# Performance work log

Measured on AMD Instinct MI355X. Metric: run time of the kernel, lower is better.

The kernel has to match this reference:

```python
import jax, jax.numpy as jnp
import numpy as np

EMBED = 1024
HEAD = 128
B, T = 4, 4096


def setup_inputs() -> dict:
    key = jax.random.key(0)
    k1, k2, k3, k4 = jax.random.split(key, 4)
    context = jax.random.normal(k1, (B, T, EMBED), dtype=jnp.float32)
    # nn.Linear(embedding_size, head_size, bias=False): y = x @ W^T; store W^T as [C, H]
    s = 1.0 / np.sqrt(EMBED)
    Wk = jax.random.normal(k2, (EMBED, HEAD), dtype=jnp.float32) * s
    Wq = jax.random.normal(k3, (EMBED, HEAD), dtype=jnp.float32) * s
    Wv = jax.random.normal(k4, (EMBED, HEAD), dtype=jnp.float32) * s
    return {"context": context, "Wk": Wk, "Wq": Wq, "Wv": Wv}


def reference(context, Wk, Wq, Wv):
    Bc, Tc, C = context.shape
    k = jnp.einsum("btc,ch->bth", context, Wk)
    q = jnp.einsum("btc,ch->bth", context, Wq)
    v = jnp.einsum("btc,ch->bth", context, Wv)
    # NOTE: original scales by 1/sqrt(C) (embedding size), not 1/sqrt(head_size)
    scale = 1.0 / jnp.sqrt(jnp.float32(C))
    scores = jnp.einsum("bqh,bkh->bqk", q, k) * scale  # [B, T, T]
    causal = jnp.tril(jnp.ones((Tc, Tc), dtype=bool))
    scores = jnp.where(causal, scores, -jnp.inf)
    attn = jax.nn.softmax(scores, axis=-1)
    # dropout_rate = 0.0 (eval-mode): no-op
    out = jnp.einsum("bqk,bkh->bqh", attn, v)
    return out
```

## Files before the change

### kernel.cpp

```cpp
#include <hip/hip_runtime.h>
#include <cstdint>
#include <cstddef>

#define EMBED 1024
#define HEAD  128
#define BATCH 4
#define SEQ   4096
#define KSC   0.04508422f

typedef __attribute__((ext_vector_type(4))) float f32x4;
typedef __attribute__((ext_vector_type(16))) float f32x16;
typedef __attribute__((ext_vector_type(8))) short s16x8;
typedef __attribute__((ext_vector_type(4))) int i32x4;
typedef __attribute__((ext_vector_type(4))) unsigned short u16x4;

__device__ __forceinline__ unsigned short f2bf(float f) {
    union { float f; unsigned u; } v; v.f = f;
    unsigned r = v.u + 0x7fffu + ((v.u >> 16) & 1u);
    return (unsigned short)(r >> 16);
}

__device__ __forceinline__ int cvtpk(float lo, float hi_) {
    int r;
    asm("v_cvt_pk_bf16_f32 %0, %1, %2" : "=v"(r) : "v"(lo), "v"(hi_));
    return r;
}

__global__ __launch_bounds__(256) void wt_kernel(const float* __restrict__ Wq,
                                                 const float* __restrict__ Wk,
                                                 const float* __restrict__ Wv,
                                                 unsigned short* __restrict__ Wt) {
    int idx = blockIdx.x * 256 + threadIdx.x;
    int sel = idx >> 17;
    int r   = idx & 131071;
    const float* W = (sel == 0) ? Wq : (sel == 1) ? Wk : Wv;
    int h = r >> 10, k = r & 1023;
    Wt[(size_t)(sel * 128 + h) * EMBED + k] = f2bf(W[(size_t)k * HEAD + h]);
}

__global__ __launch_bounds__(256) void proj_kernel(const float* __restrict__ ctx,
                                                   const unsigned short* __restrict__ Wt,
                                                   unsigned short* __restrict__ QKV) {
    __shared__ __align__(16) short As[128 * 72];
    __shared__ __align__(16) short Bs[128 * 72];
    const int tid = threadIdx.x;
    const int lane = tid & 63, w = tid >> 6;
    const int wr = w >> 1, wc = w & 1;
    const int lr = lane & 15, lk = lane >> 4;
    const int m0 = blockIdx.x * 128;
    const unsigned short* Wts = Wt + (size_t)blockIdx.y * 131072;
    unsigned short* outp = QKV + (size_t)blockIdx.y * 2097152;

    f32x4 zero = {0.f, 0.f, 0.f, 0.f};
    f32x4 acc[4][4];
    #pragma unroll
    for (int i = 0; i < 4; ++i)
        #pragma unroll
        for (int jn = 0; jn < 4; ++jn) acc[i][jn] = zero;

    for (int kk = 0; kk < EMBED; kk += 64) {
        __syncthreads();
        #pragma unroll
        for (int t = 0; t < 4; ++t) {
            int c = tid + t * 256;
            int row = c >> 3, cg = c & 7;
            const float* src = ctx + (size_t)(m0 + row) * EMBED + kk + cg * 8;
            f32x4 x0 = *(const f32x4*)src;
            f32x4 x1 = *(const f32x4*)(src + 4);
            s16x8 cv;
            cv[0] = (short)f2bf(x0[0]); cv[1] = (short)f2bf(x0[1]);
            cv[2] = (short)f2bf(x0[2]); cv[3] = (short)f2bf(x0[3]);
            cv[4] = (short)f2bf(x1[0]); cv[5] = (short)f2bf(x1[1]);
            cv[6] = (short)f2bf(x1[2]); cv[7] = (short)f2bf(x1[3]);
            *(s16x8*)&As[row * 72 + cg * 8] = cv;
            *(s16x8*)&Bs[row * 72 + cg * 8] =
                *(const s16x8*)(Wts + (size_t)row * EMBED + kk + cg * 8);
        }
        __syncthreads();
        s16x8 af[4][2], bfr[4][2];
        #pragma unroll
        for (int mi = 0; mi < 4; ++mi)
            #pragma unroll
            for (int k2 = 0; k2 < 2; ++k2)
                af[mi][k2] = *(const s16x8*)&As[(wr * 64 + mi * 16 + lr) * 72 + k2 * 32 + lk * 8];
        #pragma unroll
        for (int ni = 0; ni < 4; ++ni)
            #pragma unroll
            for (int k2 = 0; k2 < 2; ++k2)
                bfr[ni][k2] = *(const s16x8*)&Bs[(wc * 64 + ni * 16 + lr) * 72 + k2 * 32 + lk * 8];
        #pragma unroll
        for (int k2 = 0; k2 < 2; ++k2)
            #pragma unroll
            for (int mi = 0; mi < 4; ++mi)
                #pragma unroll
                for (int ni = 0; ni < 4; ++ni)
                    acc[mi][ni] = __builtin_amdgcn_mfma_f32_16x16x32_bf16(af[mi][k2], bfr[ni][k2], acc[mi][ni], 0, 0, 0);
    }
    #pragma unroll
    for (int mi = 0; mi < 4; ++mi) {
        int row = m0 + wr * 64 + mi * 16 + lk * 4;
        #pragma unroll
        for (int ni = 0; ni < 4; ++ni) {
            int col = wc * 64 + ni * 16 + lr;
            #pragma unroll
            for (int r = 0; r < 4; ++r)
                outp[(size_t)(row + r) * HEAD + col] = f2bf(acc[mi][ni][r]);
        }
    }
}

__global__ __launch_bounds__(256) void vt_kernel(const unsigned short* __restrict__ V,
                                                 unsigned short* __restrict__ Vt) {
    __shared__ __align__(16) unsigned short L[64][136];
    const int tid = threadIdx.x;
    const int t0 = blockIdx.x * 64;
    const int b  = t0 >> 12;
    const int tl = t0 & (SEQ - 1);
    #pragma unroll
    for (int j = 0; j < 4; ++j) {
        int c = tid + j * 256;
        int row = c >> 4, cg = c & 15;
        *(s16x8*)&L[row][cg * 8] =
            *(const s16x8*)(V + (size_t)(t0 + row) * HEAD + cg * 8);
    }
    __syncthreads();
    #pragma unroll
    for (int j = 0; j < 4; ++j) {
        int c = tid + j * 256;
        int h = c >> 3, tg = c & 7;
        s16x8 y;
        #pragma unroll
        for (int e = 0; e < 8; ++e) y[e] = (short)L[tg * 8 + e][h];
        *(s16x8*)(Vt + ((size_t)b * HEAD + h) * SEQ + tl + tg * 8) = y;
    }
}

__global__ __launch_bounds__(256, 2) void attn_kernel(const unsigned short* __restrict__ Q,
                                                      const unsigned short* __restrict__ K,
                                                      const unsigned short* __restrict__ Vt,
                                                      unsigned short* __restrict__ po,
                                                      float* __restrict__ pml) {
    __shared__ __align__(16) char smem[32768];
    const int tid = threadIdx.x;
    const int lane = tid & 63, w = tid >> 6;
    const int l31 = lane & 31, hi = lane >> 5;
    const int hi16 = hi << 4;

    const int b = blockIdx.x / 272;
    int t = blockIdx.x % 272;
    int qt = 0, cum = 0;
    while (cum + ((qt >> 1) + 1) <= t) { cum += (qt >> 1) + 1; ++qt; }
    const int c = t - cum;
    const int nj = min(4, 2 * qt + 2 - 4 * c);
    const int kb0 = c * 256;
    const int slot = b * 272 + cum + c;

    const unsigned short* qp = Q + ((size_t)(b * SEQ + qt * 128 + w * 32 + l31)) * HEAD + hi * 8;
    s16x8 qf[8];
    #pragma unroll
    for (int dt = 0; dt < 8; ++dt) qf[dt] = *(const s16x8*)(qp + dt * 16);

    f32x16 o0, o1, o2, o3;
    #pragma unroll
    for (int r = 0; r < 16; ++r) { o0[r] = 0.f; o1[r] = 0.f; o2[r] = 0.f; o3[r] = 0.f; }
    float m_run = -1e30f, l_run = 0.f;

    const int krow = tid >> 4, kch = tid & 15;
    const int vdr  = tid >> 3, vch = tid & 7;

    s16x8 kst[4], vst[4];
    #pragma unroll
    for (int p = 0; p < 4; ++p) {
        kst[p] = *(const s16x8*)(K + ((size_t)(b * SEQ + kb0 + krow + p * 16)) * HEAD + kch * 8);
        vst[p] = *(const s16x8*)(Vt + ((size_t)(b * HEAD + vdr + p * 32)) * SEQ + kb0 + vch * 8);
    }
    #pragma unroll
    for (int p = 0; p < 4; ++p) {
        int r0 = krow + p * 16;
        *(s16x8*)(smem + r0 * 256 + ((kch * 16) ^ ((r0 & 7) << 4))) = kst[p];
        int d0 = vdr + p * 32;
        *(s16x8*)(smem + 16384 + d0 * 128 + ((vch * 16) ^ ((d0 & 7) << 4))) = vst[p];
    }
    __syncthreads();

    for (int j = 0; j < nj; ++j) {
        const int kb = kb0 + j * 64;
        if (j + 1 < nj) {
            int kbn = kb + 64;
            #pragma unroll
            for (int p = 0; p < 4; ++p) {
                kst[p] = *(const s16x8*)(K + ((size_t)(b * SEQ + kbn + krow + p * 16)) * HEAD + kch * 8);
                vst[p] = *(const s16x8*)(Vt + ((size_t)(b * HEAD + vdr + p * 32)) * SEQ + kbn + vch * 8);
            }
        }

        f32x16 st0, st1;
        #pragma unroll
        for (int r = 0; r < 16; ++r) { st0[r] = 0.f; st1[r] = 0.f; }
        const int sw = (l31 & 7) << 4;
        const char* kbase0 = smem + l31 * 256;
        const char* kbase1 = kbase0 + 32 * 256;
        __builtin_amdgcn_s_setprio(1);
        #pragma unroll
        for (int dt = 0; dt < 8; ++dt) {
            s16x8 ka0 = *(const s16x8*)(kbase0 + ((dt * 32 + hi16) ^ sw));
            s16x8 ka1 = *(const s16x8*)(kbase1 + ((dt * 32 + hi16) ^ sw));
            st0 = __builtin_amdgcn_mfma_f32_32x32x16_bf16(ka0, qf[dt], st0, 0, 0, 0);
            st1 = __builtin_amdgcn_mfma_f32_32x32x16_bf16(ka1, qf[dt], st1, 0, 0, 0);
        }
        __builtin_amdgcn_s_setprio(0);

        if (4 * c + j >= 2 * qt) {
            const int qg = qt * 128 + w * 32 + l31;
            #pragma unroll
            for (int r = 0; r < 16; ++r) {
                int crow = (r & 3) + 8 * (r >> 2) + 4 * hi;
                if (kb + crow > qg)      st0[r] = -3e37f;
                if (kb + 32 + crow > qg) st1[r] = -3e37f;
            }
        }

        float mx = st0[0];
        #pragma unroll
        for (int r = 1; r < 16; ++r) mx = fmaxf(mx, st0[r]);
        #pragma unroll
        for (int r = 0; r < 16; ++r) mx = fmaxf(mx, st1[r]);
        mx = fmaxf(mx, __shfl_xor(mx, 32));
        float mt = mx * KSC;
        if (!__all(mt <= m_run + 8.0f)) {
            float mn = fmaxf(m_run, mt);
            float f = exp2f(m_run - mn);
            l_run *= f;
            int fi = __float_as_int(f);
            #pragma unroll
            for (int r = 0; r < 16; ++r) {
                int srcb = 4 * ((r & 3) + 8 * (r >> 2)) + 16 * hi;
                float fr = __int_as_float(__builtin_amdgcn_ds_bpermute(srcb, fi));
                o0[r] *= fr; o1[r] *= fr; o2[r] *= fr; o3[r] *= fr;
            }
            m_run = mn;
        }
        float rs = 0.f;
        #pragma unroll
        for (int r = 0; r < 16; ++r) {
            st0[r] = exp2f(fmaf(st0[r], KSC, -m_run)); rs += st0[r];
            st1[r] = exp2f(fmaf(st1[r], KSC, -m_run)); rs += st1[r];
        }
        rs += __shfl_xor(rs, 32);
        l_run += rs;

        int a0 = cvtpk(st0[0], st0[1]),   b0 = cvtpk(st0[4], st0[5]);
        int a1 = cvtpk(st0[2], st0[3]),   b1 = cvtpk(st0[6], st0[7]);
        int a2 = cvtpk(st0[8], st0[9]),   b2 = cvtpk(st0[12], st0[13]);
        int a3 = cvtpk(st0[10], st0[11]), b3 = cvtpk(st0[14], st0[15]);
        int a4 = cvtpk(st1[0], st1[1]),   b4 = cvtpk(st1[4], st1[5]);
        int a5 = cvtpk(st1[2], st1[3]),   b5 = cvtpk(st1[6], st1[7]);
        int a6 = cvtpk(st1[8], st1[9]),   b6 = cvtpk(st1[12], st1[13]);
        int a7 = cvtpk(st1[10], st1[11]), b7 = cvtpk(st1[14], st1[15]);
        asm volatile("v_permlane32_swap_b32 %0, %1" : "+v"(a0), "+v"(b0));
        asm volatile("v_permlane32_swap_b32 %0, %1" : "+v"(a1), "+v"(b1));
        asm volatile("v_permlane32_swap_b32 %0, %1" : "+v"(a2), "+v"(b2));
        asm volatile("v_permlane32_swap_b32 %0, %1" : "+v"(a3), "+v"(b3));
        asm volatile("v_permlane32_swap_b32 %0, %1" : "+v"(a4), "+v"(b4));
        asm volatile("v_permlane32_swap_b32 %0, %1" : "+v"(a5), "+v"(b5));
        asm volatile("v_permlane32_swap_b32 %0, %1" : "+v"(a6), "+v"(b6));
        asm volatile("v_permlane32_swap_b32 %0, %1" : "+v"(a7), "+v"(b7));
        i32x4 pw0 = {a0, a1, b0, b1}; s16x8 pa0 = *(s16x8*)&pw0;
        i32x4 pw1 = {a2, a3, b2, b3}; s16x8 pa1 = *(s16x8*)&pw1;
        i32x4 pw2 = {a4, a5, b4, b5}; s16x8 pa2 = *(s16x8*)&pw2;
        i32x4 pw3 = {a6, a7, b6, b7}; s16x8 pa3 = *(s16x8*)&pw3;

        __builtin_amdgcn_s_setprio(1);
        #define PV_NT(oo, nt) { \
            const int vr = (nt) * 32 + l31; \
            const int vsw = (vr & 7) << 4; \
            const char* vb = smem + 16384 + vr * 128; \
            oo = __builtin_amdgcn_mfma_f32_32x32x16_bf16(pa0, *(const s16x8*)(vb + ((0  + hi16) ^ vsw)), oo, 0, 0, 0); \
            oo = __builtin_amdgcn_mfma_f32_32x32x16_bf16(pa1, *(const s16x8*)(vb + ((32 + hi16) ^ vsw)), oo, 0, 0, 0); \
            oo = __builtin_amdgcn_mfma_f32_32x32x16_bf16(pa2, *(const s16x8*)(vb + ((64 + hi16) ^ vsw)), oo, 0, 0, 0); \
            oo = __builtin_amdgcn_mfma_f32_32x32x16_bf16(pa3, *(const s16x8*)(vb + ((96 + hi16) ^ vsw)), oo, 0, 0, 0); }
        PV_NT(o0, 0) PV_NT(o1, 1) PV_NT(o2, 2) PV_NT(o3, 3)
        #undef PV_NT
        __builtin_amdgcn_s_setprio(0);

        if (j + 1 < nj) {
            __syncthreads();
            #pragma unroll
            for (int p = 0; p < 4; ++p) {
                int r0 = krow + p * 16;
                *(s16x8*)(smem + r0 * 256 + ((kch * 16) ^ ((r0 & 7) << 4))) = kst[p];
                int d0 = vdr + p * 32;
                *(s16x8*)(smem + 16384 + d0 * 128 + ((vch * 16) ^ ((d0 & 7) << 4))) = vst[p];
            }
            __syncthreads();
        }
    }

    unsigned short* pob = po + (size_t)slot * 16384;
    #define STORE_NT(oo, nt) { \
        _Pragma("unroll") \
        for (int r = 0; r < 16; ++r) { \
            int qin = w * 32 + (r & 3) + 8 * (r >> 2) + 4 * hi; \
            pob[qin * 128 + (nt) * 32 + l31] = f2bf(oo[r]); \
        } }
    STORE_NT(o0, 0) STORE_NT(o1, 1) STORE_NT(o2, 2) STORE_NT(o3, 3)
    #undef STORE_NT
    if (lane < 32) {
        float* pm = pml + (size_t)slot * 256 + (w * 32 + lane) * 2;
        pm[0] = m_run; pm[1] = l_run;
    }
}

__global__ __launch_bounds__(256) void combine_kernel(const unsigned short* __restrict__ po,
                                                      const float* __restrict__ pml,
                                                      float* __restrict__ out) {
    const int tid = threadIdx.x;
    const int row = blockIdx.x * 8 + (tid >> 5);
    const int l32 = tid & 31;
    const int b = row >> 12, q = row & 4095;
    const int qt = q >> 7, qr = q & 127;
    const int nc = (q >> 8) + 1;
    const int cum = ((qt >> 1) + (qt & 1)) * ((qt >> 1) + 1);
    const size_t bslot = (size_t)b * 272 + cum;

    float M = -1e30f;
    for (int cc = 0; cc < nc; ++cc)
        M = fmaxf(M, pml[(bslot + cc) * 256 + qr * 2]);
    float L = 0.f;
    f32x4 acc = {0.f, 0.f, 0.f, 0.f};
    for (int cc = 0; cc < nc; ++cc) {
        const float* pm = pml + (bslot + cc) * 256 + qr * 2;
        float wgt = exp2f(pm[0] - M);
        L += wgt * pm[1];
        u16x4 x = *(const u16x4*)(po + (bslot + cc) * 16384 + qr * 128 + l32 * 4);
        #pragma unroll
        for (int e = 0; e < 4; ++e) {
            union { unsigned u; float f; } cv; cv.u = ((unsigned)x[e]) << 16;
            acc[e] += wgt * cv.f;
        }
    }
    float inv = 1.f / L;
    f32x4 y = {acc[0] * inv, acc[1] * inv, acc[2] * inv, acc[3] * inv};
    *(f32x4*)(out + (size_t)row * HEAD + l32 * 4) = y;
}

extern "C" void kernel_launch(void* const* d_in, const int* in_sizes, int n_in,
                              void* d_out, int out_size, void* d_ws, size_t ws_size,
                              hipStream_t stream) {
    const float* ctx = (const float*)d_in[0];
    const float* Wk  = (const float*)d_in[1];
    const float* Wq  = (const float*)d_in[2];
    const float* Wv  = (const float*)d_in[3];
    float* out = (float*)d_out;

    unsigned short* Wt  = (unsigned short*)d_ws;
    unsigned short* Qb  = Wt + 3 * 131072;
    unsigned short* Kb  = Qb + 2097152;
    unsigned short* Vb  = Kb + 2097152;
    unsigned short* Vtb = Vb + 2097152;
    unsigned short* po  = Vtb + 2097152;
    float* pml = (float*)(po + (size_t)1088 * 16384);

    wt_kernel<<<1536, 256, 0, stream>>>(Wq, Wk, Wv, Wt);
    proj_kernel<<<dim3(128, 3), 256, 0, stream>>>(ctx, Wt, Qb);
    vt_kernel<<<256, 256, 0, stream>>>(Vb, Vtb);
    attn_kernel<<<1088, 256, 0, stream>>>(Qb, Kb, Vtb, po, pml);
    combine_kernel<<<2048, 256, 0, stream>>>(po, pml, out);
}
```

Before: 176.6 us.

## Fuse V transpose into projection, prescale Q, tile weight transpose, halve proj M-tile

The projection kernel now writes V directly in transposed layout, so the separate vt_kernel launch and its extra global round trip go away. Q is pre-multiplied by the softmax scale (log2e/sqrt(C)) before bf16 rounding, which removes a multiply per score in the attention inner loop. The weight transpose kernel now uses a shared-memory tile with coalesced vector loads and stores and hardware bf16 packing. The projection M-tile shrinks to 64 rows, doubling the grid for better occupancy. Folding the scale into Q before rounding to bf16 changes rounding slightly, and the transposed V stores are 8-byte scattered writes.

```diff
diff --git a/kernel.cpp b/kernel.cpp
--- a/kernel.cpp
+++ b/kernel.cpp
@@ -30,59 +30,84 @@
                                                  const float* __restrict__ Wk,
                                                  const float* __restrict__ Wv,
                                                  unsigned short* __restrict__ Wt) {
-    int idx = blockIdx.x * 256 + threadIdx.x;
-    int sel = idx >> 17;
-    int r   = idx & 131071;
+    __shared__ __align__(16) float Lw[32 * 132];
+    const int tid = threadIdx.x;
+    const int sel = blockIdx.x >> 5;
+    const int k0  = (blockIdx.x & 31) * 32;
     const float* W = (sel == 0) ? Wq : (sel == 1) ? Wk : Wv;
-    int h = r >> 10, k = r & 1023;
-    Wt[(size_t)(sel * 128 + h) * EMBED + k] = f2bf(W[(size_t)k * HEAD + h]);
+    #pragma unroll
+    for (int t = 0; t < 4; ++t) {
+        int c = tid + t * 256;
+        int kk = c >> 5, hc = c & 31;
+        *(f32x4*)&Lw[kk * 132 + hc * 4] =
+            *(const f32x4*)(W + (size_t)(k0 + kk) * HEAD + hc * 4);
+    }
+    __syncthreads();
+    #pragma unroll
+    for (int t = 0; t < 2; ++t) {
+        int c = tid + t * 256;
+        int h = c >> 2, cg = c & 3;
+        int p0 = cvtpk(Lw[(cg * 8 + 0) * 132 + h], Lw[(cg * 8 + 1) * 132 + h]);
+        int p1 = cvtpk(Lw[(cg * 8 + 2) * 132 + h], Lw[(cg * 8 + 3) * 132 + h]);
+        int p2 = cvtpk(Lw[(cg * 8 + 4) * 132 + h], Lw[(cg * 8 + 5) * 132 + h]);
+        int p3 = cvtpk(Lw[(cg * 8 + 6) * 132 + h], Lw[(cg * 8 + 7) * 132 + h]);
+        i32x4 pk = {p0, p1, p2, p3};
+        *(s16x8*)(Wt + (size_t)(sel * 128 + h) * EMBED + k0 + cg * 8) = *(s16x8*)&pk;
+    }
 }
 
 __global__ __launch_bounds__(256) void proj_kernel(const float* __restrict__ ctx,
                                                    const unsigned short* __restrict__ Wt,
-                                                   unsigned short* __restrict__ QKV) {
-    __shared__ __align__(16) short As[128 * 72];
+                                                   unsigned short* __restrict__ Qb,
+                                                   unsigned short* __restrict__ Kb,
+                                                   unsigned short* __restrict__ Vtb) {
+    __shared__ __align__(16) short As[64 * 72];
     __shared__ __align__(16) short Bs[128 * 72];
     const int tid = threadIdx.x;
     const int lane = tid & 63, w = tid >> 6;
     const int wr = w >> 1, wc = w & 1;
     const int lr = lane & 15, lk = lane >> 4;
-    const int m0 = blockIdx.x * 128;
-    const unsigned short* Wts = Wt + (size_t)blockIdx.y * 131072;
-    unsigned short* outp = QKV + (size_t)blockIdx.y * 2097152;
+    const int m0 = blockIdx.x * 64;
+    const int sel = blockIdx.y;
+    const unsigned short* Wts = Wt + (size_t)sel * 131072;
 
     f32x4 zero = {0.f, 0.f, 0.f, 0.f};
-    f32x4 acc[4][4];
-    #pragma unroll
-    for (int i = 0; i < 4; ++i)
+    f32x4 acc[2][4];
+    #pragma unroll
+    for (int i = 0; i < 2; ++i)
         #pragma unroll
         for (int jn = 0; jn < 4; ++jn) acc[i][jn] = zero;
 
     for (int kk = 0; kk < EMBED; kk += 64) {
         __syncthreads();
         #pragma unroll
-        for (int t = 0; t < 4; ++t) {
+        for (int t = 0; t < 2; ++t) {
             int c = tid + t * 256;
             int row = c >> 3, cg = c & 7;
             const float* src = ctx + (size_t)(m0 + row) * EMBED + kk + cg * 8;
             f32x4 x0 = *(const f32x4*)src;
             f32x4 x1 = *(const f32x4*)(src + 4);
-            s16x8 cv;
-            cv[0] = (short)f2bf(x0[0]); cv[1] = (short)f2bf(x0[1]);
-            cv[2] = (short)f2bf(x0[2]); cv[3] = (short)f2bf(x0[3]);
-            cv[4] = (short)f2bf(x1[0]); cv[5] = (short)f2bf(x1[1]);
-            cv[6] = (short)f2bf(x1[2]); cv[7] = (short)f2bf(x1[3]);
-            *(s16x8*)&As[row * 72 + cg * 8] = cv;
+            int p0 = cvtpk(x0[0], x0[1]);
+            int p1 = cvtpk(x0[2], x0[3]);
+            int p2 = cvtpk(x1[0], x1[1]);
+            int p3 = cvtpk(x1[2], x1[3]);
+            i32x4 pk = {p0, p1, p2, p3};
+            *(s16x8*)&As[row * 72 + cg * 8] = *(s16x8*)&pk;
+        }
+        #pragma unroll
+        for (int t = 0; t < 4; ++t) {
+            int c = tid + t * 256;
+            int row = c >> 3, cg = c & 7;
             *(s16x8*)&Bs[row * 72 + cg * 8] =
                 *(const s16x8*)(Wts + (size_t)row * EMBED + kk + cg * 8);
         }
         __syncthreads();
-        s16x8 af[4][2], bfr[4][2];
-        #pragma unroll
-        for (int mi = 0; mi < 4; ++mi)
+        s16x8 af[2][2], bfr[4][2];
+        #pragma unroll
+        for (int mi = 0; mi < 2; ++mi)
             #pragma unroll
             for (int k2 = 0; k2 < 2; ++k2)
-                af[mi][k2] = *(const s16x8*)&As[(wr * 64 + mi * 16 + lr) * 72 + k2 * 32 + lk * 8];
+                af[mi][k2] = *(const s16x8*)&As[(wr * 32 + mi * 16 + lr) * 72 + k2 * 32 + lk * 8];
         #pragma unroll
         for (int ni = 0; ni < 4; ++ni)
             #pragma unroll
@@ -91,47 +116,40 @@
         #pragma unroll
         for (int k2 = 0; k2 < 2; ++k2)
             #pragma unroll
-            for (int mi = 0; mi < 4; ++mi)
+            for (int mi = 0; mi < 2; ++mi)
                 #pragma unroll
                 for (int ni = 0; ni < 4; ++ni)
                     acc[mi][ni] = __builtin_amdgcn_mfma_f32_16x16x32_bf16(af[mi][k2], bfr[ni][k2], acc[mi][ni], 0, 0, 0);
     }
-    #pragma unroll
-    for (int mi = 0; mi < 4; ++mi) {
-        int row = m0 + wr * 64 + mi * 16 + lk * 4;
-        #pragma unroll
-        for (int ni = 0; ni < 4; ++ni) {
-            int col = wc * 64 + ni * 16 + lr;
-            #pragma unroll
-            for (int r = 0; r < 4; ++r)
-                outp[(size_t)(row + r) * HEAD + col] = f2bf(acc[mi][ni][r]);
-        }
-    }
-}
-
-__global__ __launch_bounds__(256) void vt_kernel(const unsigned short* __restrict__ V,
-                                                 unsigned short* __restrict__ Vt) {
-    __shared__ __align__(16) unsigned short L[64][136];
-    const int tid = threadIdx.x;
-    const int t0 = blockIdx.x * 64;
-    const int b  = t0 >> 12;
-    const int tl = t0 & (SEQ - 1);
-    #pragma unroll
-    for (int j = 0; j < 4; ++j) {
-        int c = tid + j * 256;
-        int row = c >> 4, cg = c & 15;
-        *(s16x8*)&L[row][cg * 8] =
-            *(const s16x8*)(V + (size_t)(t0 + row) * HEAD + cg * 8);
-    }
-    __syncthreads();
-    #pragma unroll
-    for (int j = 0; j < 4; ++j) {
-        int c = tid + j * 256;
-        int h = c >> 3, tg = c & 7;
-        s16x8 y;
-        #pragma unroll
-        for (int e = 0; e < 8; ++e) y[e] = (short)L[tg * 8 + e][h];
-        *(s16x8*)(Vt + ((size_t)b * HEAD + h) * SEQ + tl + tg * 8) = y;
+
+    if (sel == 2) {
+        #pragma unroll
+        for (int mi = 0; mi < 2; ++mi) {
+            int t0r = m0 + wr * 32 + mi * 16 + lk * 4;
+            int b = t0r >> 12, tl = t0r & (SEQ - 1);
+            #pragma unroll
+            for (int ni = 0; ni < 4; ++ni) {
+                int col = wc * 64 + ni * 16 + lr;
+                u16x4 vv;
+                #pragma unroll
+                for (int r = 0; r < 4; ++r) vv[r] = f2bf(acc[mi][ni][r]);
+                *(u16x4*)(Vtb + ((size_t)(b * HEAD + col)) * SEQ + tl) = vv;
+            }
+        }
+    } else {
+        unsigned short* outp = sel ? Kb : Qb;
+        const float sc = sel ? 1.0f : KSC;
+        #pragma unroll
+        for (int mi = 0; mi < 2; ++mi) {
+            int row = m0 + wr * 32 + mi * 16 + lk * 4;
+            #pragma unroll
+            for (int ni = 0; ni < 4; ++ni) {
+                int col = wc * 64 + ni * 16 + lr;
+                #pragma unroll
+                for (int r = 0; r < 4; ++r)
+                    outp[(size_t)(row + r) * HEAD + col] = f2bf(acc[mi][ni][r] * sc);
+            }
+        }
     }
 }
 
@@ -226,9 +244,8 @@
         #pragma unroll
         for (int r = 0; r < 16; ++r) mx = fmaxf(mx, st1[r]);
         mx = fmaxf(mx, __shfl_xor(mx, 32));
-        float mt = mx * KSC;
-        if (!__all(mt <= m_run + 8.0f)) {
-            float mn = fmaxf(m_run, mt);
+        if (!__all(mx <= m_run + 8.0f)) {
+            float mn = fmaxf(m_run, mx);
             float f = exp2f(m_run - mn);
             l_run *= f;
             int fi = __float_as_int(f);
@@ -243,8 +260,8 @@
         float rs = 0.f;
         #pragma unroll
         for (int r = 0; r < 16; ++r) {
-            st0[r] = exp2f(fmaf(st0[r], KSC, -m_run)); rs += st0[r];
-            st1[r] = exp2f(fmaf(st1[r], KSC, -m_run)); rs += st1[r];
+            st0[r] = exp2f(st0[r] - m_run); rs += st0[r];
+            st1[r] = exp2f(st1[r] - m_run); rs += st1[r];
         }
         rs += __shfl_xor(rs, 32);
         l_run += rs;
@@ -356,14 +373,12 @@
     unsigned short* Wt  = (unsigned short*)d_ws;
     unsigned short* Qb  = Wt + 3 * 131072;
     unsigned short* Kb  = Qb + 2097152;
-    unsigned short* Vb  = Kb + 2097152;
-    unsigned short* Vtb = Vb + 2097152;
+    unsigned short* Vtb = Kb + 2097152;
     unsigned short* po  = Vtb + 2097152;
     float* pml = (float*)(po + (size_t)1088 * 16384);
 
-    wt_kernel<<<1536, 256, 0, stream>>>(Wq, Wk, Wv, Wt);
-    proj_kernel<<<dim3(128, 3), 256, 0, stream>>>(ctx, Wt, Qb);
-    vt_kernel<<<256, 256, 0, stream>>>(Vb, Vtb);
+    wt_kernel<<<96, 256, 0, stream>>>(Wq, Wk, Wv, Wt);
+    proj_kernel<<<dim3(256, 3), 256, 0, stream>>>(ctx, Wt, Qb, Kb, Vtb);
     attn_kernel<<<1088, 256, 0, stream>>>(Qb, Kb, Vtb, po, pml);
     combine_kernel<<<2048, 256, 0, stream>>>(po, pml, out);
 }
```

Measured after the change: 163.5 us. 7.4% less time.
